# Optimization experiments

Measured on AMD Instinct MI355X. Metric: run time of the kernel, lower is better.

## Reference

```python
import jax, jax.numpy as jnp
import numpy as np

B, T, C = 4, 2048, 1024
H = 16
D = C // H  # head_dim = 64


def setup_inputs() -> dict:
    key = jax.random.key(0)
    ks = jax.random.split(key, 9)
    s = 1.0 / np.sqrt(C)
    return {
        "x": jax.random.normal(ks[0], (B, T, C), dtype=jnp.float32),
        "Wk": jax.random.uniform(ks[1], (C, C), jnp.float32, -s, s),
        "bk": jax.random.uniform(ks[2], (C,), jnp.float32, -s, s),
        "Wq": jax.random.uniform(ks[3], (C, C), jnp.float32, -s, s),
        "bq": jax.random.uniform(ks[4], (C,), jnp.float32, -s, s),
        "Wv": jax.random.uniform(ks[5], (C, C), jnp.float32, -s, s),
        "bv": jax.random.uniform(ks[6], (C,), jnp.float32, -s, s),
        "Wp": jax.random.uniform(ks[7], (C, C), jnp.float32, -s, s),
        "bp": jax.random.uniform(ks[8], (C,), jnp.float32, -s, s),
    }


def reference(x, Wk, bk, Wq, bq, Wv, bv, Wp, bp):
    # projections -> (B, H, T, D)
    def split_heads(y):
        return y.reshape(B, T, H, D).transpose(0, 2, 1, 3)

    k = split_heads(x @ Wk.T + bk)
    q = split_heads(x @ Wq.T + bq)
    v = split_heads(x @ Wv.T + bv)

    att = jnp.einsum("bhtd,bhsd->bhts", q, k) / np.sqrt(D).astype(np.float32)
    causal = jnp.tril(jnp.ones((T, T), dtype=bool))
    att = jnp.where(causal, att, -jnp.inf)
    att = jax.nn.softmax(att, axis=-1)

    y = jnp.einsum("bhts,bhsd->bhtd", att, v)  # (B,H,T,D)
    y = y.transpose(0, 2, 1, 3).reshape(B, T, C)
    return y @ Wp.T + bp
```

## Files before the change

### kernel.cpp

```cpp
#include <hip/hip_runtime.h>
#include <hip/hip_bf16.h>

typedef unsigned short u16;
typedef unsigned int u32;
typedef short short8 __attribute__((ext_vector_type(8)));
typedef short short4v __attribute__((ext_vector_type(4)));
typedef float f32x4 __attribute__((ext_vector_type(4)));
typedef unsigned int u32x4 __attribute__((ext_vector_type(4)));

#define MFMA16(a, b, c) __builtin_amdgcn_mfma_f32_16x16x32_bf16((a), (b), (c), 0, 0, 0)

constexpr int kB = 4, kT = 2048, kC = 1024, kH = 16, kD = 64;
constexpr int kBT = kB * kT;
constexpr long kQKV = (long)kB * kH * kT * kD;
constexpr float kSC = 0.125f * 1.4426950408889634f;

__device__ inline u16 f2bf(float f) {
    __hip_bfloat16 h = __float2bfloat16(f);
    return *reinterpret_cast<u16*>(&h);
}
__device__ inline u32 pkbf_trunc(float lo, float hi) {
    return __builtin_amdgcn_perm(__builtin_bit_cast(u32, hi),
                                 __builtin_bit_cast(u32, lo), 0x07060302u);
}
__device__ inline u32 pkbf_rne(float lo, float hi) {
    return ((u32)f2bf(hi) << 16) | (u32)f2bf(lo);
}

__device__ inline void cp16(const u16* g, u16* l) {
    __builtin_amdgcn_global_load_lds(
        (const __attribute__((address_space(1))) unsigned int*)g,
        (__attribute__((address_space(3))) unsigned int*)l, 16, 0, 0);
}

__global__ __launch_bounds__(256) void cast_kernel(
    const float* __restrict__ x,  const float* __restrict__ Wk,
    const float* __restrict__ Wq, const float* __restrict__ Wv,
    const float* __restrict__ Wp,
    u16* __restrict__ xb, u16* __restrict__ wkb, u16* __restrict__ wqb,
    u16* __restrict__ wvb, u16* __restrict__ wpb)
{
    const long id = (long)blockIdx.x * 256 + threadIdx.x;
    const float* src;
    u16* dst;
    long off;
    if (id < 2097152) {
        src = x; dst = xb; off = id;
    } else {
        const long w = (id - 2097152) >> 18;
        off = (id - 2097152) & 262143;
        src = (w == 0) ? Wk : (w == 1) ? Wq : (w == 2) ? Wv : Wp;
        dst = (w == 0) ? wkb : (w == 1) ? wqb : (w == 2) ? wvb : wpb;
    }
    f32x4 v = *(const f32x4*)&src[off * 4];
    short4v s = {(short)f2bf(v[0]), (short)f2bf(v[1]),
                 (short)f2bf(v[2]), (short)f2bf(v[3])};
    *(short4v*)&dst[off * 4] = s;
}


__global__ __launch_bounds__(512, 1) void qkv_gemm_bf16(
    const u16* __restrict__ xb, const u16* __restrict__ wall,
    const float* __restrict__ bk, const float* __restrict__ bq,
    const float* __restrict__ bv,
    u16* __restrict__ kw, u16* __restrict__ qw, u16* __restrict__ vw)
{
    __shared__ __align__(16) u16 A2[2][128 * 64];
    __shared__ __align__(16) u16 B2[2][256 * 64];

    const int tid = threadIdx.x;
    const int lane = tid & 63;
    const int wid = tid >> 6;
    const int l15 = lane & 15;
    const int quad = lane >> 4;
    const int wr = wid & 1;
    const int wc = wid >> 1;
    const int m0 = blockIdx.x * 128;
    const int n0c = blockIdx.y * 256;

    f32x4 zero = {0.f, 0.f, 0.f, 0.f};
    f32x4 acc[4][4];
#pragma unroll
    for (int i = 0; i < 4; ++i)
#pragma unroll
        for (int j = 0; j < 4; ++j) acc[i][j] = zero;

    const int vA = tid >> 3, chA = tid & 7;
    const int rowMa = ((vA >> 5) << 6) + (vA & 31);
    const int rowMb = rowMa + 32;
    const u16* aMaS = xb + (long)(m0 + rowMa) * kC + ((chA ^ (rowMa & 7)) * 8);
    const u16* aMbS = xb + (long)(m0 + rowMb) * kC + ((chA ^ (rowMb & 7)) * 8);
    const int aMaD = rowMa * 64 + chA * 8;
    const int aMbD = rowMb * 64 + chA * 8;
    const u16* bNaS[2]; const u16* bNbS[2];
    int bNaD[2], bNbD[2];
#pragma unroll
    for (int q = 0; q < 2; ++q) {
        const int slot = q * 512 + tid;
        const int v = slot >> 3, ch = slot & 7;
        const int ra = ((v >> 5) << 6) + (v & 31);
        const int rb = ra + 32;
        bNaS[q] = wall + (long)(n0c + ra) * kC + ((ch ^ (ra & 7)) * 8);
        bNbS[q] = wall + (long)(n0c + rb) * kC + ((ch ^ (rb & 7)) * 8);
        bNaD[q] = ra * 64 + ch * 8;
        bNbD[q] = rb * 64 + ch * 8;
    }

    int aOff[4][2], bOff[4][2];
#pragma unroll
    for (int i = 0; i < 4; ++i) {
        const int row = wr * 64 + i * 16 + l15;
#pragma unroll
        for (int k2 = 0; k2 < 2; ++k2)
            aOff[i][k2] = row * 64 + (((k2 * 4 + quad) ^ (row & 7)) * 8);
    }
#pragma unroll
    for (int j = 0; j < 4; ++j) {
        const int row = wc * 64 + j * 16 + l15;
#pragma unroll
        for (int k2 = 0; k2 < 2; ++k2)
            bOff[j][k2] = row * 64 + (((k2 * 4 + quad) ^ (row & 7)) * 8);
    }

    cp16(bNaS[0], &B2[0][bNaD[0]]);
    cp16(bNaS[1], &B2[0][bNaD[1]]);
    cp16(aMaS,    &A2[0][aMaD]);
    cp16(aMbS,    &A2[0][aMbD]);
    cp16(bNbS[0], &B2[0][bNbD[0]]);
    cp16(bNbS[1], &B2[0][bNbD[1]]);

#pragma unroll 2
    for (int t = 0; t < 16; ++t) {
        const int c = t & 1;
        const u16* Ab = A2[c];
        const u16* Bb = B2[c];
        u16* An = A2[c ^ 1];
        u16* Bn = B2[c ^ 1];
        const long ko = (long)(t + 1) * 64;
        const bool pf = (t < 15);

        short8 amL[2][2], amH[2][2], bnL[2][2], bnH[2][2];

        asm volatile("s_waitcnt vmcnt(2)" ::: "memory");
        __builtin_amdgcn_s_barrier();
        __builtin_amdgcn_sched_barrier(0);
#pragma unroll
        for (int i = 0; i < 2; ++i)
#pragma unroll
            for (int k2 = 0; k2 < 2; ++k2)
                amL[i][k2] = *(const short8*)&Ab[aOff[i][k2]];
#pragma unroll
        for (int j = 0; j < 2; ++j)
#pragma unroll
            for (int k2 = 0; k2 < 2; ++k2)
                bnL[j][k2] = *(const short8*)&Bb[bOff[j][k2]];
        if (pf) {
            cp16(bNaS[0] + ko, &Bn[bNaD[0]]);
            cp16(bNaS[1] + ko, &Bn[bNaD[1]]);
        }
        asm volatile("s_waitcnt lgkmcnt(0)" ::: "memory");
        __builtin_amdgcn_sched_barrier(0);
        __builtin_amdgcn_s_setprio(1);
#pragma unroll
        for (int i = 0; i < 2; ++i)
#pragma unroll
            for (int j = 0; j < 2; ++j) {
                acc[i][j] = MFMA16(amL[i][0], bnL[j][0], acc[i][j]);
                acc[i][j] = MFMA16(amL[i][1], bnL[j][1], acc[i][j]);
            }
        __builtin_amdgcn_s_setprio(0);

#pragma unroll
        for (int i = 0; i < 2; ++i)
#pragma unroll
            for (int k2 = 0; k2 < 2; ++k2)
                amH[i][k2] = *(const short8*)&Ab[aOff[2 + i][k2]];
        if (pf) {
            cp16(aMaS + ko, &An[aMaD]);
            cp16(aMbS + ko, &An[aMbD]);
        }
        asm volatile("s_waitcnt lgkmcnt(0)" ::: "memory");
        __builtin_amdgcn_sched_barrier(0);
        __builtin_amdgcn_s_setprio(1);
#pragma unroll
        for (int i = 0; i < 2; ++i)
#pragma unroll
            for (int j = 0; j < 2; ++j) {
                acc[2 + i][j] = MFMA16(amH[i][0], bnL[j][0], acc[2 + i][j]);
                acc[2 + i][j] = MFMA16(amH[i][1], bnL[j][1], acc[2 + i][j]);
            }
        __builtin_amdgcn_s_setprio(0);

        if (pf) {
            asm volatile("s_waitcnt vmcnt(4)" ::: "memory");
        } else {
            asm volatile("s_waitcnt vmcnt(0)" ::: "memory");
        }
        __builtin_amdgcn_s_barrier();
        __builtin_amdgcn_sched_barrier(0);
#pragma unroll
        for (int j = 0; j < 2; ++j)
#pragma unroll
            for (int k2 = 0; k2 < 2; ++k2)
                bnH[j][k2] = *(const short8*)&Bb[bOff[2 + j][k2]];
        if (pf) {
            cp16(bNbS[0] + ko, &Bn[bNbD[0]]);
            cp16(bNbS[1] + ko, &Bn[bNbD[1]]);
        }
        asm volatile("s_waitcnt lgkmcnt(0)" ::: "memory");
        __builtin_amdgcn_sched_barrier(0);
        __builtin_amdgcn_s_setprio(1);
#pragma unroll
        for (int i = 0; i < 2; ++i)
#pragma unroll
            for (int j = 0; j < 2; ++j) {
                acc[i][2 + j] = MFMA16(amL[i][0], bnH[j][0], acc[i][2 + j]);
                acc[i][2 + j] = MFMA16(amL[i][1], bnH[j][1], acc[i][2 + j]);
            }
        __builtin_amdgcn_s_setprio(0);

        __builtin_amdgcn_s_setprio(1);
#pragma unroll
        for (int i = 0; i < 2; ++i)
#pragma unroll
            for (int j = 0; j < 2; ++j) {
                acc[2 + i][2 + j] = MFMA16(amH[i][0], bnH[j][0], acc[2 + i][2 + j]);
                acc[2 + i][2 + j] = MFMA16(amH[i][1], bnH[j][1], acc[2 + i][2 + j]);
            }
        __builtin_amdgcn_s_setprio(0);
    }

    const int z = (n0c >> 10);
    const float scale = (z == 1) ? kSC : 1.0f;
    const float* bias = (z == 0) ? bk : (z == 1) ? bq : bv;
#pragma unroll
    for (int j = 0; j < 4; ++j) {
        const int n = n0c + wc * 64 + j * 16 + l15;
        const int np = n & 1023;
        const float bias_f = bias[np];
        const int h = np >> 6, d = np & 63;
#pragma unroll
        for (int i = 0; i < 4; ++i) {
#pragma unroll
            for (int r = 0; r < 4; ++r) {
                const int m = m0 + wr * 64 + i * 16 + quad * 4 + r;
                const int b = m >> 11, tt = m & 2047;
                const float v = (acc[i][j][r] + bias_f) * scale;
                const int bh = b * kH + h;
                if (z == 2) {
                    vw[((long)bh * kD + d) * kT + tt] = f2bf(v);
                } else {
                    u16* dst = (z == 0) ? kw : qw;
                    dst[((long)bh * kT + tt) * kD + d] = f2bf(v);
                }
            }
        }
    }
}

__global__ __launch_bounds__(256) void qkv_gemm_kernel(
    const float* __restrict__ x,
    const float* __restrict__ Wk, const float* __restrict__ bk,
    const float* __restrict__ Wq, const float* __restrict__ bq,
    const float* __restrict__ Wv, const float* __restrict__ bv,
    u16* __restrict__ kw, u16* __restrict__ qw, u16* __restrict__ vw)
{
    __shared__ u16 As[128 * 32];
    __shared__ u16 Bs[128 * 32];
    const int tid = threadIdx.x;
    const int lane = tid & 63;
    const int wid = tid >> 6;
    const int l15 = lane & 15;
    const int quad = lane >> 4;
    const int m0 = blockIdx.x * 128;
    const int n0 = blockIdx.y * 128;
    const int z = blockIdx.z;

    const float* W = (z == 0) ? Wk : (z == 1) ? Wq : Wv;
    const float* bias = (z == 0) ? bk : (z == 1) ? bq : bv;

    f32x4 zero = {0.f, 0.f, 0.f, 0.f};
    f32x4 acc[4][4];
#pragma unroll
    for (int i = 0; i < 4; ++i)
#pragma unroll
        for (int j = 0; j < 4; ++j) acc[i][j] = zero;

    const int wm = (wid & 1) * 64;
    const int wn = (wid >> 1) * 64;
    const int row4 = tid >> 3;
    const int col4 = (tid & 7) * 4;

    for (int k0 = 0; k0 < kC; k0 += 32) {
#pragma unroll
        for (int p = 0; p < 4; ++p) {
            const int r = p * 32 + row4;
            f32x4 xa = *(const f32x4*)&x[(long)(m0 + r) * kC + k0 + col4];
            f32x4 wa = *(const f32x4*)&W[(long)(n0 + r) * kC + k0 + col4];
            short4v xs = {(short)f2bf(xa[0]), (short)f2bf(xa[1]),
                          (short)f2bf(xa[2]), (short)f2bf(xa[3])};
            short4v wsv = {(short)f2bf(wa[0]), (short)f2bf(wa[1]),
                           (short)f2bf(wa[2]), (short)f2bf(wa[3])};
            *(short4v*)&As[r * 32 + col4] = xs;
            *(short4v*)&Bs[r * 32 + col4] = wsv;
        }
        __syncthreads();
        short8 af[4], bfr[4];
#pragma unroll
        for (int mt = 0; mt < 4; ++mt)
            af[mt] = *(const short8*)&As[(wm + mt * 16 + l15) * 32 + quad * 8];
#pragma unroll
        for (int nt = 0; nt < 4; ++nt)
            bfr[nt] = *(const short8*)&Bs[(wn + nt * 16 + l15) * 32 + quad * 8];
#pragma unroll
        for (int mt = 0; mt < 4; ++mt)
#pragma unroll
            for (int nt = 0; nt < 4; ++nt)
                acc[mt][nt] = MFMA16(af[mt], bfr[nt], acc[mt][nt]);
        __syncthreads();
    }

    const float scale = (z == 1) ? kSC : 1.0f;
#pragma unroll
    for (int nt = 0; nt < 4; ++nt) {
        const int n = n0 + wn + nt * 16 + l15;
        const float bias_f = bias[n];
        const int h = n >> 6, d = n & 63;
#pragma unroll
        for (int mt = 0; mt < 4; ++mt) {
#pragma unroll
            for (int r = 0; r < 4; ++r) {
                const int m = m0 + wm + mt * 16 + quad * 4 + r;
                const int b = m >> 11, t = m & 2047;
                const float v = (acc[mt][nt][r] + bias_f) * scale;
                const int bh = b * kH + h;
                if (z == 2) {
                    vw[((long)bh * kD + d) * kT + t] = f2bf(v);
                } else {
                    u16* dst = (z == 0) ? kw : qw;
                    dst[((long)bh * kT + t) * kD + d] = f2bf(v);
                }
            }
        }
    }
}

__global__ __launch_bounds__(256, 4) void attn_kernel(
    const u16* qw, const u16* kw, const u16* vw, u16* ow)
{
    __shared__ u16 Ks[2][64 * 64];
    __shared__ u16 VT[2][64 * 64];

    const int tid = threadIdx.x;
    const int lane = tid & 63;
    const int wid = tid >> 6;
    const int l15 = lane & 15;
    const int quad = lane >> 4;
    const int id = blockIdx.x;
    const int bh = id & 63;
    constexpr int pperm[16] = {15, 14, 13, 12, 0, 1, 2, 3,
                               11, 10, 9, 8, 4, 5, 6, 7};
    const int p = pperm[id >> 6];
    const int p2 = 2 * p;
    const int n_st = p2 + 2;
    const int tw = p * 128 + wid * 32;

    const float NEG = -1.0e30f;
    f32x4 zero = {0.f, 0.f, 0.f, 0.f};
    const short8 onesf = {(short)0x3F80, (short)0x3F80, (short)0x3F80, (short)0x3F80,
                          (short)0x3F80, (short)0x3F80, (short)0x3F80, (short)0x3F80};

    const int rl7 = l15 & 7;

    const u16* kbase = kw + (long)bh * kT * kD;
    const u16* vbase = vw + (long)bh * kD * kT;

    const u16* kp[2];
    const u16* vp[2];
    int sdst[2];
#pragma unroll
    for (int q = 0; q < 2; ++q) {
        const int slot = q * 256 + tid;
        const int row = slot >> 3;
        const int c = slot & 7;
        const int off = (c ^ (row & 7)) * 8;
        kp[q] = kbase + (long)row * kD + off;
        vp[q] = vbase + (long)row * kT + off;
        sdst[q] = slot * 8;
    }

    auto stage = [&](int buf, int st) {
        u16* kd = Ks[buf];
        u16* vd = VT[buf];
#pragma unroll
        for (int q = 0; q < 2; ++q) {
            cp16(kp[q] + (long)st * (64 * kD), kd + sdst[q]);
            cp16(vp[q] + st * 64,              vd + sdst[q]);
        }
    };

    short8 qf[2][2];
#pragma unroll
    for (int g = 0; g < 2; ++g) {
        const u16* qp = qw + ((long)bh * kT + tw + g * 16 + l15) * kD;
        qf[g][0] = *(const short8*)&qp[quad * 8];
        qf[g][1] = *(const short8*)&qp[32 + quad * 8];
    }

    stage(0, 0);
    stage(1, 1);
    __syncthreads();

    f32x4 oacc[4][2];
#pragma unroll
    for (int mo = 0; mo < 4; ++mo)
#pragma unroll
        for (int g = 0; g < 2; ++g) oacc[mo][g] = zero;
    f32x4 lsum[2] = {zero, zero};

    for (int st = 0; st < n_st; ++st) {
        const int cur = st & 1;
        const u16* K_ = Ks[cur];
        const u16* V_ = VT[cur];

        f32x4 sacc[4][2];
        __builtin_amdgcn_s_setprio(1);
#pragma unroll
        for (int ms = 0; ms < 4; ++ms) {
            const int row = ms * 16 + l15;
            short8 kf0 = *(const short8*)&K_[row * 64 + ((quad ^ rl7) * 8)];
            short8 kf1 = *(const short8*)&K_[row * 64 + (((4 + quad) ^ rl7) * 8)];
#pragma unroll
            for (int g = 0; g < 2; ++g) {
                sacc[ms][g] = MFMA16(kf0, qf[g][0], zero);
                sacc[ms][g] = MFMA16(kf1, qf[g][1], sacc[ms][g]);
            }
        }
        __builtin_amdgcn_s_setprio(0);

        const int dg = st - p2;
        if (dg >= 0) {
#pragma unroll
            for (int g = 0; g < 2; ++g) {
                const int off = wid * 32 + g * 16 + l15 - dg * 64;
#pragma unroll
                for (int ms = 0; ms < 4; ++ms)
#pragma unroll
                    for (int r = 0; r < 4; ++r)
                        if (ms * 16 + quad * 4 + r > off) sacc[ms][g][r] = NEG;
            }
        }

        short8 pfr[2][2];
#pragma unroll
        for (int g = 0; g < 2; ++g) {
#pragma unroll
            for (int k2 = 0; k2 < 2; ++k2) {
                const int msA = k2 * 2, msB = k2 * 2 + 1;
                const float a0 = exp2f(sacc[msA][g][0]);
                const float a1 = exp2f(sacc[msA][g][1]);
                const float a2 = exp2f(sacc[msA][g][2]);
                const float a3 = exp2f(sacc[msA][g][3]);
                const float b0 = exp2f(sacc[msB][g][0]);
                const float b1 = exp2f(sacc[msB][g][1]);
                const float b2 = exp2f(sacc[msB][g][2]);
                const float b3 = exp2f(sacc[msB][g][3]);
                const u32 LA = pkbf_trunc(a0, a1), HA = pkbf_trunc(a2, a3);
                const u32 LB = pkbf_trunc(b0, b1), HB = pkbf_trunc(b2, b3);
                auto pL = __builtin_amdgcn_permlane32_swap(LA, LB, false, false);
                auto pH = __builtin_amdgcn_permlane32_swap(HA, HB, false, false);
                auto rL = __builtin_amdgcn_permlane16_swap(pL[0], pL[1], false, false);
                auto rH = __builtin_amdgcn_permlane16_swap(pH[0], pH[1], false, false);
                u32x4 w;
                w[0] = rL[0]; w[1] = rH[0]; w[2] = rL[1]; w[3] = rH[1];
                pfr[g][k2] = __builtin_bit_cast(short8, w);
            }
        }

#pragma unroll
        for (int g = 0; g < 2; ++g) {
            lsum[g] = MFMA16(onesf, pfr[g][0], lsum[g]);
            lsum[g] = MFMA16(onesf, pfr[g][1], lsum[g]);
        }

        __builtin_amdgcn_s_setprio(1);
#pragma unroll
        for (int mo = 0; mo < 4; ++mo) {
            const int row = mo * 16 + l15;
            short8 vf0 = *(const short8*)&V_[row * 64 + ((quad ^ rl7) * 8)];
            short8 vf1 = *(const short8*)&V_[row * 64 + (((4 + quad) ^ rl7) * 8)];
#pragma unroll
            for (int g = 0; g < 2; ++g) {
                oacc[mo][g] = MFMA16(vf0, pfr[g][0], oacc[mo][g]);
                oacc[mo][g] = MFMA16(vf1, pfr[g][1], oacc[mo][g]);
            }
        }
        __builtin_amdgcn_s_setprio(0);

        if (st + 1 < n_st) {
            __syncthreads();
            if (st + 2 < n_st) stage(cur, st + 2);
        }
    }

#pragma unroll
    for (int g = 0; g < 2; ++g) {
        const float inv = 1.0f / lsum[g][0];
        const int t = tw + g * 16 + l15;
        u16* op = ow + ((long)bh * kT + t) * kD;
#pragma unroll
        for (int mo = 0; mo < 4; ++mo) {
            uint2 ov;
            ov.x = pkbf_rne(oacc[mo][g][0] * inv, oacc[mo][g][1] * inv);
            ov.y = pkbf_rne(oacc[mo][g][2] * inv, oacc[mo][g][3] * inv);
            *(uint2*)&op[mo * 16 + quad * 4] = ov;
        }
    }
}

__global__ __launch_bounds__(512, 1) void out_gemm_bf16(
    const u16* __restrict__ ob, const u16* __restrict__ wpb,
    const float* __restrict__ bp, float* __restrict__ out)
{
    __shared__ __align__(16) u16 A2[2][128 * 64];
    __shared__ __align__(16) u16 B2[2][256 * 64];

    const int tid = threadIdx.x;
    const int lane = tid & 63;
    const int wid = tid >> 6;
    const int l15 = lane & 15;
    const int quad = lane >> 4;
    const int wr = wid & 1;
    const int wc = wid >> 1;
    const int m0 = blockIdx.x * 128;
    const int n0 = blockIdx.y * 256;

    f32x4 zero = {0.f, 0.f, 0.f, 0.f};
    f32x4 acc[4][4];
#pragma unroll
    for (int i = 0; i < 4; ++i)
#pragma unroll
        for (int j = 0; j < 4; ++j) acc[i][j] = zero;

    const int vA = tid >> 3, chA = tid & 7;
    const int rowMa = ((vA >> 5) << 6) + (vA & 31);
    const int rowMb = rowMa + 32;
    const int mMa = m0 + rowMa, mMb = m0 + rowMb;
    const u16* aMaS = ob + (((long)(mMa >> 11) * kH) * kT + (mMa & 2047)) * kD
                      + ((chA ^ (rowMa & 7)) * 8);
    const u16* aMbS = ob + (((long)(mMb >> 11) * kH) * kT + (mMb & 2047)) * kD
                      + ((chA ^ (rowMb & 7)) * 8);
    const int aMaD = rowMa * 64 + chA * 8;
    const int aMbD = rowMb * 64 + chA * 8;

    const u16* bNaS[2]; const u16* bNbS[2];
    int bNaD[2], bNbD[2];
#pragma unroll
    for (int q = 0; q < 2; ++q) {
        const int slot = q * 512 + tid;
        const int v = slot >> 3, ch = slot & 7;
        const int ra = ((v >> 5) << 6) + (v & 31);
        const int rb = ra + 32;
        bNaS[q] = wpb + (long)(n0 + ra) * kC + ((ch ^ (ra & 7)) * 8);
        bNbS[q] = wpb + (long)(n0 + rb) * kC + ((ch ^ (rb & 7)) * 8);
        bNaD[q] = ra * 64 + ch * 8;
        bNbD[q] = rb * 64 + ch * 8;
    }

    int aOff[4][2], bOff[4][2];
#pragma unroll
    for (int i = 0; i < 4; ++i) {
        const int row = wr * 64 + i * 16 + l15;
#pragma unroll
        for (int k2 = 0; k2 < 2; ++k2)
            aOff[i][k2] = row * 64 + (((k2 * 4 + quad) ^ (row & 7)) * 8);
    }
#pragma unroll
    for (int j = 0; j < 4; ++j) {
        const int row = wc * 64 + j * 16 + l15;
#pragma unroll
        for (int k2 = 0; k2 < 2; ++k2)
            bOff[j][k2] = row * 64 + (((k2 * 4 + quad) ^ (row & 7)) * 8);
    }

    cp16(bNaS[0], &B2[0][bNaD[0]]);
    cp16(bNaS[1], &B2[0][bNaD[1]]);
    cp16(aMaS,    &A2[0][aMaD]);
    cp16(aMbS,    &A2[0][aMbD]);
    cp16(bNbS[0], &B2[0][bNbD[0]]);
    cp16(bNbS[1], &B2[0][bNbD[1]]);

#pragma unroll 2
    for (int t = 0; t < 16; ++t) {
        const int c = t & 1;
        const u16* Ab = A2[c];
        const u16* Bb = B2[c];
        u16* An = A2[c ^ 1];
        u16* Bn = B2[c ^ 1];
        const long koA = (long)(t + 1) * kT * kD;
        const long koB = (long)(t + 1) * 64;
        const bool pf = (t < 15);

        short8 amL[2][2], amH[2][2], bnL[2][2], bnH[2][2];

        asm volatile("s_waitcnt vmcnt(2)" ::: "memory");
        __builtin_amdgcn_s_barrier();
        __builtin_amdgcn_sched_barrier(0);
#pragma unroll
        for (int i = 0; i < 2; ++i)
#pragma unroll
            for (int k2 = 0; k2 < 2; ++k2)
                amL[i][k2] = *(const short8*)&Ab[aOff[i][k2]];
#pragma unroll
        for (int j = 0; j < 2; ++j)
#pragma unroll
            for (int k2 = 0; k2 < 2; ++k2)
                bnL[j][k2] = *(const short8*)&Bb[bOff[j][k2]];
        if (pf) {
            cp16(bNaS[0] + koB, &Bn[bNaD[0]]);
            cp16(bNaS[1] + koB, &Bn[bNaD[1]]);
        }
        asm volatile("s_waitcnt lgkmcnt(0)" ::: "memory");
        __builtin_amdgcn_sched_barrier(0);
        __builtin_amdgcn_s_setprio(1);
#pragma unroll
        for (int i = 0; i < 2; ++i)
#pragma unroll
            for (int j = 0; j < 2; ++j) {
                acc[i][j] = MFMA16(amL[i][0], bnL[j][0], acc[i][j]);
                acc[i][j] = MFMA16(amL[i][1], bnL[j][1], acc[i][j]);
            }
        __builtin_amdgcn_s_setprio(0);

#pragma unroll
        for (int i = 0; i < 2; ++i)
#pragma unroll
            for (int k2 = 0; k2 < 2; ++k2)
                amH[i][k2] = *(const short8*)&Ab[aOff[2 + i][k2]];
        if (pf) {
            cp16(aMaS + koA, &An[aMaD]);
            cp16(aMbS + koA, &An[aMbD]);
        }
        asm volatile("s_waitcnt lgkmcnt(0)" ::: "memory");
        __builtin_amdgcn_sched_barrier(0);
        __builtin_amdgcn_s_setprio(1);
#pragma unroll
        for (int i = 0; i < 2; ++i)
#pragma unroll
            for (int j = 0; j < 2; ++j) {
                acc[2 + i][j] = MFMA16(amH[i][0], bnL[j][0], acc[2 + i][j]);
                acc[2 + i][j] = MFMA16(amH[i][1], bnL[j][1], acc[2 + i][j]);
            }
        __builtin_amdgcn_s_setprio(0);

        if (pf) {
            asm volatile("s_waitcnt vmcnt(4)" ::: "memory");
        } else {
            asm volatile("s_waitcnt vmcnt(0)" ::: "memory");
        }
        __builtin_amdgcn_s_barrier();
        __builtin_amdgcn_sched_barrier(0);
#pragma unroll
        for (int j = 0; j < 2; ++j)
#pragma unroll
            for (int k2 = 0; k2 < 2; ++k2)
                bnH[j][k2] = *(const short8*)&Bb[bOff[2 + j][k2]];
        if (pf) {
            cp16(bNbS[0] + koB, &Bn[bNbD[0]]);
            cp16(bNbS[1] + koB, &Bn[bNbD[1]]);
        }
        asm volatile("s_waitcnt lgkmcnt(0)" ::: "memory");
        __builtin_amdgcn_sched_barrier(0);
        __builtin_amdgcn_s_setprio(1);
#pragma unroll
        for (int i = 0; i < 2; ++i)
#pragma unroll
            for (int j = 0; j < 2; ++j) {
                acc[i][2 + j] = MFMA16(amL[i][0], bnH[j][0], acc[i][2 + j]);
                acc[i][2 + j] = MFMA16(amL[i][1], bnH[j][1], acc[i][2 + j]);
            }
        __builtin_amdgcn_s_setprio(0);

        __builtin_amdgcn_s_setprio(1);
#pragma unroll
        for (int i = 0; i < 2; ++i)
#pragma unroll
            for (int j = 0; j < 2; ++j) {
                acc[2 + i][2 + j] = MFMA16(amH[i][0], bnH[j][0], acc[2 + i][2 + j]);
                acc[2 + i][2 + j] = MFMA16(amH[i][1], bnH[j][1], acc[2 + i][2 + j]);
            }
        __builtin_amdgcn_s_setprio(0);
    }

#pragma unroll
    for (int j = 0; j < 4; ++j) {
        const int n = n0 + wc * 64 + j * 16 + l15;
        const float bias_f = bp[n];
#pragma unroll
        for (int i = 0; i < 4; ++i) {
#pragma unroll
            for (int r = 0; r < 4; ++r) {
                const int m = m0 + wr * 64 + i * 16 + quad * 4 + r;
                out[(long)m * kC + n] = acc[i][j][r] + bias_f;
            }
        }
    }
}

__global__ __launch_bounds__(256) void out_gemm_kernel(
    const u16* __restrict__ ow, const float* __restrict__ Wp,
    const float* __restrict__ bp, float* __restrict__ out)
{
    __shared__ u16 As[128 * 32];
    __shared__ u16 Bs[128 * 32];
    const int tid = threadIdx.x;
    const int lane = tid & 63;
    const int wid = tid >> 6;
    const int l15 = lane & 15;
    const int quad = lane >> 4;
    const int m0 = blockIdx.x * 128;
    const int n0 = blockIdx.y * 128;

    f32x4 zero = {0.f, 0.f, 0.f, 0.f};
    f32x4 acc[4][4];
#pragma unroll
    for (int i = 0; i < 4; ++i)
#pragma unroll
        for (int j = 0; j < 4; ++j) acc[i][j] = zero;

    const int wm = (wid & 1) * 64;
    const int wn = (wid >> 1) * 64;

    const int r0 = tid >> 2;
    const int kkA = (tid & 3) * 8;
    const int r1 = r0 + 64;
    const int row4 = tid >> 3;
    const int col4 = (tid & 7) * 4;

    for (int k0 = 0; k0 < kC; k0 += 32) {
        {
            const int m = m0 + r0, b = m >> 11, t = m & 2047;
            const int kk = k0 + kkA, h = kk >> 6, d = kk & 63;
            *(short8*)&As[r0 * 32 + kkA] =
                *(const short8*)&ow[(((long)b * kH + h) * kT + t) * kD + d];
        }
        {
            const int m = m0 + r1, b = m >> 11, t = m & 2047;
            const int kk = k0 + kkA, h = kk >> 6, d = kk & 63;
            *(short8*)&As[r1 * 32 + kkA] =
                *(const short8*)&ow[(((long)b * kH + h) * kT + t) * kD + d];
        }
#pragma unroll
        for (int p = 0; p < 4; ++p) {
            const int r = p * 32 + row4;
            f32x4 wa = *(const f32x4*)&Wp[(long)(n0 + r) * kC + k0 + col4];
            short4v wsv = {(short)f2bf(wa[0]), (short)f2bf(wa[1]),
                           (short)f2bf(wa[2]), (short)f2bf(wa[3])};
            *(short4v*)&Bs[r * 32 + col4] = wsv;
        }
        __syncthreads();
        short8 af[4], bfr[4];
#pragma unroll
        for (int mt = 0; mt < 4; ++mt)
            af[mt] = *(const short8*)&As[(wm + mt * 16 + l15) * 32 + quad * 8];
#pragma unroll
        for (int nt = 0; nt < 4; ++nt)
            bfr[nt] = *(const short8*)&Bs[(wn + nt * 16 + l15) * 32 + quad * 8];
#pragma unroll
        for (int mt = 0; mt < 4; ++mt)
#pragma unroll
            for (int nt = 0; nt < 4; ++nt)
                acc[mt][nt] = MFMA16(af[mt], bfr[nt], acc[mt][nt]);
        __syncthreads();
    }

#pragma unroll
    for (int nt = 0; nt < 4; ++nt) {
        const int n = n0 + wn + nt * 16 + l15;
        const float bias_f = bp[n];
#pragma unroll
        for (int mt = 0; mt < 4; ++mt) {
#pragma unroll
            for (int r = 0; r < 4; ++r) {
                const int m = m0 + wm + mt * 16 + quad * 4 + r;
                out[(long)m * kC + n] = acc[mt][nt][r] + bias_f;
            }
        }
    }
}

extern "C" void kernel_launch(void* const* d_in, const int* in_sizes, int n_in,
                              void* d_out, int out_size, void* d_ws, size_t ws_size,
                              hipStream_t stream) {
    const float* x  = (const float*)d_in[0];
    const float* Wk = (const float*)d_in[1];
    const float* bk = (const float*)d_in[2];
    const float* Wq = (const float*)d_in[3];
    const float* bq = (const float*)d_in[4];
    const float* Wv = (const float*)d_in[5];
    const float* bv = (const float*)d_in[6];
    const float* Wp = (const float*)d_in[7];
    const float* bp = (const float*)d_in[8];
    float* out = (float*)d_out;

    u16* ws = (u16*)d_ws;
    const size_t kNeed = 72ull * 1024 * 1024;

    if (ws_size >= kNeed) {
        u16* k_ws = ws;
        u16* q_ws = ws + kQKV;
        u16* v_ws = ws + 2 * kQKV;
        u16* xb   = ws + 3 * kQKV;
        u16* o_ws = xb;
        u16* wkb  = ws + 4 * kQKV;
        u16* wqb  = wkb + (long)kC * kC;
        u16* wvb  = wqb + (long)kC * kC;
        u16* wpb  = wvb + (long)kC * kC;

        cast_kernel<<<12288, 256, 0, stream>>>(x, Wk, Wq, Wv, Wp,
                                               xb, wkb, wqb, wvb, wpb);
        qkv_gemm_bf16<<<dim3(kBT / 128, 12), 512, 0, stream>>>(
            xb, wkb, bk, bq, bv, k_ws, q_ws, v_ws);
        attn_kernel<<<1024, 256, 0, stream>>>(q_ws, k_ws, v_ws, o_ws);
        out_gemm_bf16<<<dim3(kBT / 128, kC / 256), 512, 0, stream>>>(
            o_ws, wpb, bp, out);
    } else {
        u16* k_ws = ws;
        u16* q_ws = ws + kQKV;
        u16* v_ws = ws + 2 * kQKV;
        u16* o_ws = q_ws;

        qkv_gemm_kernel<<<dim3(kBT / 128, kC / 128, 3), 256, 0, stream>>>(
            x, Wk, bk, Wq, bq, Wv, bv, k_ws, q_ws, v_ws);
        attn_kernel<<<1024, 256, 0, stream>>>(q_ws, k_ws, v_ws, o_ws);
        out_gemm_kernel<<<dim3(kBT / 128, kC / 128), 256, 0, stream>>>(
            o_ws, Wp, bp, out);
    }
}
```

Measured before the change: 251.0 us.

## Shrink GEMM tiles to 128x128 with 256-thread blocks, two per CU

Both bf16 GEMMs (QKV and output projection) move from 128x256 tiles on 512-thread blocks to 128x128 tiles on 256-thread blocks, with launch bounds set to allow two blocks per CU. The grid doubles in the N dimension and each thread now issues twice as many A-tile async copies, with the vmcnt wait thresholds adjusted to match. The aim is better occupancy and wave balance across CUs, at the cost of less data reuse per tile and more global and L2 traffic for the A operand.

```diff
diff --git a/kernel.cpp b/kernel.cpp
--- a/kernel.cpp
+++ b/kernel.cpp
@@ -59,14 +59,14 @@
 }
 
 
-__global__ __launch_bounds__(512, 1) void qkv_gemm_bf16(
+__global__ __launch_bounds__(256, 2) void qkv_gemm_bf16(
     const u16* __restrict__ xb, const u16* __restrict__ wall,
     const float* __restrict__ bk, const float* __restrict__ bq,
     const float* __restrict__ bv,
     u16* __restrict__ kw, u16* __restrict__ qw, u16* __restrict__ vw)
 {
     __shared__ __align__(16) u16 A2[2][128 * 64];
-    __shared__ __align__(16) u16 B2[2][256 * 64];
+    __shared__ __align__(16) u16 B2[2][128 * 64];
 
     const int tid = threadIdx.x;
     const int lane = tid & 63;
@@ -76,7 +76,7 @@
     const int wr = wid & 1;
     const int wc = wid >> 1;
     const int m0 = blockIdx.x * 128;
-    const int n0c = blockIdx.y * 256;
+    const int n0c = blockIdx.y * 128;
 
     f32x4 zero = {0.f, 0.f, 0.f, 0.f};
     f32x4 acc[4][4];
@@ -85,21 +85,19 @@
 #pragma unroll
         for (int j = 0; j < 4; ++j) acc[i][j] = zero;
 
-    const int vA = tid >> 3, chA = tid & 7;
-    const int rowMa = ((vA >> 5) << 6) + (vA & 31);
-    const int rowMb = rowMa + 32;
-    const u16* aMaS = xb + (long)(m0 + rowMa) * kC + ((chA ^ (rowMa & 7)) * 8);
-    const u16* aMbS = xb + (long)(m0 + rowMb) * kC + ((chA ^ (rowMb & 7)) * 8);
-    const int aMaD = rowMa * 64 + chA * 8;
-    const int aMbD = rowMb * 64 + chA * 8;
+    const u16* aMaS[2]; const u16* aMbS[2];
     const u16* bNaS[2]; const u16* bNbS[2];
-    int bNaD[2], bNbD[2];
+    int aMaD[2], aMbD[2], bNaD[2], bNbD[2];
 #pragma unroll
     for (int q = 0; q < 2; ++q) {
-        const int slot = q * 512 + tid;
+        const int slot = q * 256 + tid;
         const int v = slot >> 3, ch = slot & 7;
         const int ra = ((v >> 5) << 6) + (v & 31);
         const int rb = ra + 32;
+        aMaS[q] = xb + (long)(m0 + ra) * kC + ((ch ^ (ra & 7)) * 8);
+        aMbS[q] = xb + (long)(m0 + rb) * kC + ((ch ^ (rb & 7)) * 8);
+        aMaD[q] = ra * 64 + ch * 8;
+        aMbD[q] = rb * 64 + ch * 8;
         bNaS[q] = wall + (long)(n0c + ra) * kC + ((ch ^ (ra & 7)) * 8);
         bNbS[q] = wall + (long)(n0c + rb) * kC + ((ch ^ (rb & 7)) * 8);
         bNaD[q] = ra * 64 + ch * 8;
@@ -124,8 +122,10 @@
 
     cp16(bNaS[0], &B2[0][bNaD[0]]);
     cp16(bNaS[1], &B2[0][bNaD[1]]);
-    cp16(aMaS,    &A2[0][aMaD]);
-    cp16(aMbS,    &A2[0][aMbD]);
+    cp16(aMaS[0], &A2[0][aMaD[0]]);
+    cp16(aMaS[1], &A2[0][aMaD[1]]);
+    cp16(aMbS[0], &A2[0][aMbD[0]]);
+    cp16(aMbS[1], &A2[0][aMbD[1]]);
     cp16(bNbS[0], &B2[0][bNbD[0]]);
     cp16(bNbS[1], &B2[0][bNbD[1]]);
 
@@ -176,8 +176,10 @@
             for (int k2 = 0; k2 < 2; ++k2)
                 amH[i][k2] = *(const short8*)&Ab[aOff[2 + i][k2]];
         if (pf) {
-            cp16(aMaS + ko, &An[aMaD]);
-            cp16(aMbS + ko, &An[aMbD]);
+            cp16(aMaS[0] + ko, &An[aMaD[0]]);
+            cp16(aMaS[1] + ko, &An[aMaD[1]]);
+            cp16(aMbS[0] + ko, &An[aMbD[0]]);
+            cp16(aMbS[1] + ko, &An[aMbD[1]]);
         }
         asm volatile("s_waitcnt lgkmcnt(0)" ::: "memory");
         __builtin_amdgcn_sched_barrier(0);
@@ -192,7 +194,7 @@
         __builtin_amdgcn_s_setprio(0);
 
         if (pf) {
-            asm volatile("s_waitcnt vmcnt(4)" ::: "memory");
+            asm volatile("s_waitcnt vmcnt(6)" ::: "memory");
         } else {
             asm volatile("s_waitcnt vmcnt(0)" ::: "memory");
         }
@@ -518,12 +520,12 @@
     }
 }
 
-__global__ __launch_bounds__(512, 1) void out_gemm_bf16(
+__global__ __launch_bounds__(256, 2) void out_gemm_bf16(
     const u16* __restrict__ ob, const u16* __restrict__ wpb,
     const float* __restrict__ bp, float* __restrict__ out)
 {
     __shared__ __align__(16) u16 A2[2][128 * 64];
-    __shared__ __align__(16) u16 B2[2][256 * 64];
+    __shared__ __align__(16) u16 B2[2][128 * 64];
 
     const int tid = threadIdx.x;
     const int lane = tid & 63;
@@ -533,7 +535,7 @@
     const int wr = wid & 1;
     const int wc = wid >> 1;
     const int m0 = blockIdx.x * 128;
-    const int n0 = blockIdx.y * 256;
+    const int n0 = blockIdx.y * 128;
 
     f32x4 zero = {0.f, 0.f, 0.f, 0.f};
     f32x4 acc[4][4];
@@ -542,25 +544,22 @@
 #pragma unroll
         for (int j = 0; j < 4; ++j) acc[i][j] = zero;
 
-    const int vA = tid >> 3, chA = tid & 7;
-    const int rowMa = ((vA >> 5) << 6) + (vA & 31);
-    const int rowMb = rowMa + 32;
-    const int mMa = m0 + rowMa, mMb = m0 + rowMb;
-    const u16* aMaS = ob + (((long)(mMa >> 11) * kH) * kT + (mMa & 2047)) * kD
-                      + ((chA ^ (rowMa & 7)) * 8);
-    const u16* aMbS = ob + (((long)(mMb >> 11) * kH) * kT + (mMb & 2047)) * kD
-                      + ((chA ^ (rowMb & 7)) * 8);
-    const int aMaD = rowMa * 64 + chA * 8;
-    const int aMbD = rowMb * 64 + chA * 8;
-
+    const u16* aMaS[2]; const u16* aMbS[2];
     const u16* bNaS[2]; const u16* bNbS[2];
-    int bNaD[2], bNbD[2];
+    int aMaD[2], aMbD[2], bNaD[2], bNbD[2];
 #pragma unroll
     for (int q = 0; q < 2; ++q) {
-        const int slot = q * 512 + tid;
+        const int slot = q * 256 + tid;
         const int v = slot >> 3, ch = slot & 7;
         const int ra = ((v >> 5) << 6) + (v & 31);
         const int rb = ra + 32;
+        const int mA = m0 + ra, mB = m0 + rb;
+        aMaS[q] = ob + (((long)(mA >> 11) * kH) * kT + (mA & 2047)) * kD
+                  + ((ch ^ (ra & 7)) * 8);
+        aMbS[q] = ob + (((long)(mB >> 11) * kH) * kT + (mB & 2047)) * kD
+                  + ((ch ^ (rb & 7)) * 8);
+        aMaD[q] = ra * 64 + ch * 8;
+        aMbD[q] = rb * 64 + ch * 8;
         bNaS[q] = wpb + (long)(n0 + ra) * kC + ((ch ^ (ra & 7)) * 8);
         bNbS[q] = wpb + (long)(n0 + rb) * kC + ((ch ^ (rb & 7)) * 8);
         bNaD[q] = ra * 64 + ch * 8;
@@ -585,8 +584,10 @@
 
     cp16(bNaS[0], &B2[0][bNaD[0]]);
     cp16(bNaS[1], &B2[0][bNaD[1]]);
-    cp16(aMaS,    &A2[0][aMaD]);
-    cp16(aMbS,    &A2[0][aMbD]);
+    cp16(aMaS[0], &A2[0][aMaD[0]]);
+    cp16(aMaS[1], &A2[0][aMaD[1]]);
+    cp16(aMbS[0], &A2[0][aMbD[0]]);
+    cp16(aMbS[1], &A2[0][aMbD[1]]);
     cp16(bNbS[0], &B2[0][bNbD[0]]);
     cp16(bNbS[1], &B2[0][bNbD[1]]);
 
@@ -638,8 +639,10 @@
             for (int k2 = 0; k2 < 2; ++k2)
                 amH[i][k2] = *(const short8*)&Ab[aOff[2 + i][k2]];
         if (pf) {
-            cp16(aMaS + koA, &An[aMaD]);
-            cp16(aMbS + koA, &An[aMbD]);
+            cp16(aMaS[0] + koA, &An[aMaD[0]]);
+            cp16(aMaS[1] + koA, &An[aMaD[1]]);
+            cp16(aMbS[0] + koA, &An[aMbD[0]]);
+            cp16(aMbS[1] + koA, &An[aMbD[1]]);
         }
         asm volatile("s_waitcnt lgkmcnt(0)" ::: "memory");
         __builtin_amdgcn_sched_barrier(0);
@@ -654,7 +657,7 @@
         __builtin_amdgcn_s_setprio(0);
 
         if (pf) {
-            asm volatile("s_waitcnt vmcnt(4)" ::: "memory");
+            asm volatile("s_waitcnt vmcnt(6)" ::: "memory");
         } else {
             asm volatile("s_waitcnt vmcnt(0)" ::: "memory");
         }
@@ -819,10 +822,10 @@
 
         cast_kernel<<<12288, 256, 0, stream>>>(x, Wk, Wq, Wv, Wp,
                                                xb, wkb, wqb, wvb, wpb);
-        qkv_gemm_bf16<<<dim3(kBT / 128, 12), 512, 0, stream>>>(
+        qkv_gemm_bf16<<<dim3(kBT / 128, 24), 256, 0, stream>>>(
             xb, wkb, bk, bq, bv, k_ws, q_ws, v_ws);
         attn_kernel<<<1024, 256, 0, stream>>>(q_ws, k_ws, v_ws, o_ws);
-        out_gemm_bf16<<<dim3(kBT / 128, kC / 256), 512, 0, stream>>>(
+        out_gemm_bf16<<<dim3(kBT / 128, kC / 128), 256, 0, stream>>>(
             o_ws, wpb, bp, out);
     } else {
         u16* k_ws = ws;
```

After: 260.5 us. 1.04x slower.
